# Optimization experiments

Measured on AMD Instinct MI355X. Metric: run time of the kernel, lower is better.

Reference implementation:

```python
import jax, jax.numpy as jnp
import numpy as np
import math

B, S, E, H = 2, 2048, 1024, 16
D = E // H
EPS = 1e-5


def setup_inputs() -> dict:
    key = jax.random.key(0)
    ks = jax.random.split(key, 6)
    s = 1.0 / math.sqrt(E)
    return {
        "query": jax.random.normal(ks[0], (B, S, E), jnp.float32),
        "Wq": jax.random.normal(ks[1], (E, E), jnp.float32) * s,
        "bq": jnp.zeros((E,), jnp.float32),
        "Wk": jax.random.normal(ks[2], (E, E), jnp.float32) * s,
        "bk": jnp.zeros((E,), jnp.float32),
        "Wv": jax.random.normal(ks[3], (E, E), jnp.float32) * s,
        "bv": jnp.zeros((E,), jnp.float32),
        "Wo": jax.random.normal(ks[4], (E, E), jnp.float32) * s,
        "bo": jnp.zeros((E,), jnp.float32),
        "alpha": jnp.ones((1,), jnp.float32),
    }


def reference(query, Wq, bq, Wk, bk, Wv, bv, Wo, bo, alpha):
    # Q/K/V projections (nn.Linear: x @ W.T + b)
    q = (query @ Wq.T + bq).reshape(B, S, H, D)
    k = (query @ Wk.T + bk).reshape(B, S, H, D)
    v = (query @ Wv.T + bv).reshape(B, S, H, D)

    # YAT scores: (q.k)^2 / (||q-k||^2 + eps)
    qk = jnp.einsum('bqhd,bkhd->bhqk', q, k)          # [B,H,S,S]
    sq = jnp.einsum('bqhd,bqhd->bhq', q, q)           # ||q||^2
    sk = jnp.einsum('bkhd,bkhd->bhk', k, k)           # ||k||^2
    dist_sq = sq[..., :, None] + sk[..., None, :] - 2.0 * qk
    scores = (qk * qk) / (dist_sq + EPS)

    # learnable alpha scaling: scores * (sqrt(d)/log(1+d))^alpha
    scale = (jnp.sqrt(jnp.float32(D)) / jnp.log1p(jnp.float32(D))) ** alpha[0]
    scores = scores * scale

    attn = jax.nn.softmax(scores, axis=-1)
    out = jnp.einsum('bhqk,bkhd->bqhd', attn, v).reshape(B, S, E)
    return out @ Wo.T + bo
```

## Files before the change

### kernel.cpp

```cpp
#include <hip/hip_runtime.h>
#include <hip/hip_fp16.h>
#include <math.h>

#define BB 2
#define SS 2048
#define EE 1024
#define HH 16
#define DD 64
#define YAT_EPS 1e-5f
#define RR (BB * HH * SS)

typedef __attribute__((ext_vector_type(8))) short bf16x8;
typedef __attribute__((ext_vector_type(4))) short short4v;
typedef __attribute__((ext_vector_type(4))) float f32x4;
#define MFMA16(a, b, c) __builtin_amdgcn_mfma_f32_16x16x32_bf16((a), (b), (c), 0, 0, 0)

#if __has_builtin(__builtin_amdgcn_exp2f)
#define EXP2(x) __builtin_amdgcn_exp2f(x)
#else
#define EXP2(x) exp2f(x)
#endif
#if __has_builtin(__builtin_amdgcn_rcpf)
#define RCPF(x) __builtin_amdgcn_rcpf(x)
#else
#define RCPF(x) (1.0f / (x))
#endif

__device__ __forceinline__ unsigned short f2bf(float x) {
    unsigned int u = __float_as_uint(x);
    u += 0x7FFFu + ((u >> 16) & 1u);
    return (unsigned short)(u >> 16);
}
__device__ __forceinline__ float bf2f(unsigned short h) {
    return __uint_as_float(((unsigned int)h) << 16);
}
__device__ __forceinline__ short f2bf_t(float x) {
    return (short)(__float_as_uint(x) >> 16);
}

__device__ __forceinline__ void async_ld16(void* lds, const void* g) {
    __builtin_amdgcn_global_load_lds(
        (const __attribute__((address_space(1))) unsigned int*)g,
        (__attribute__((address_space(3))) unsigned int*)lds, 16, 0, 0);
}

__global__ __launch_bounds__(256) void split_all(
        const float* __restrict__ x,
        const float* __restrict__ Wq, const float* __restrict__ Wk,
        const float* __restrict__ Wv, const float* __restrict__ Wo,
        unsigned short* __restrict__ xhi, unsigned short* __restrict__ xlo,
        unsigned short* __restrict__ Whi, unsigned short* __restrict__ Wlo,
        unsigned short* __restrict__ Wohi) {
    const int bid = blockIdx.x;
    if (bid < 4096) {
        int i = bid * 256 + threadIdx.x;
        float4 v = ((const float4*)x)[i];
        ushort4 h, l;
        h.x = f2bf(v.x); l.x = f2bf(v.x - bf2f(h.x));
        h.y = f2bf(v.y); l.y = f2bf(v.y - bf2f(h.y));
        h.z = f2bf(v.z); l.z = f2bf(v.z - bf2f(h.z));
        h.w = f2bf(v.w); l.w = f2bf(v.w - bf2f(h.w));
        ((ushort4*)xhi)[i] = h;
        ((ushort4*)xlo)[i] = l;
    } else {
        int idx = bid - 4096;
        int y = idx >> 10;
        int i = (idx & 1023) * 256 + threadIdx.x;
        const float* src = y == 0 ? Wq : y == 1 ? Wk : y == 2 ? Wv : Wo;
        unsigned short* hi = y < 3 ? Whi + (size_t)y * EE * EE : Wohi;
        float4 v = ((const float4*)src)[i];
        ushort4 h;
        h.x = f2bf(v.x); h.y = f2bf(v.y); h.z = f2bf(v.z); h.w = f2bf(v.w);
        ((ushort4*)hi)[i] = h;
        if (y < 2) {
            unsigned short* lo = Wlo + (size_t)y * EE * EE;
            ushort4 l;
            l.x = f2bf(v.x - bf2f(h.x));
            l.y = f2bf(v.y - bf2f(h.y));
            l.z = f2bf(v.z - bf2f(h.z));
            l.w = f2bf(v.w - bf2f(h.w));
            ((ushort4*)lo)[i] = l;
        }
    }
}

__global__ __launch_bounds__(256, 2) void proj_qkv(
        const unsigned short* __restrict__ Ahi, const unsigned short* __restrict__ Alo,
        const unsigned short* __restrict__ Whi, const unsigned short* __restrict__ Wlo,
        const float* __restrict__ bq, const float* __restrict__ bk,
        const float* __restrict__ bv,
        unsigned short* __restrict__ qhi, unsigned short* __restrict__ qlo,
        unsigned short* __restrict__ khi, unsigned short* __restrict__ vt,
        float* __restrict__ sqn, float* __restrict__ skn) {
    __shared__ __align__(16) unsigned short SH[128 * 136];
    unsigned short* LA_hi = SH;
    unsigned short* LA_lo = SH + 4096;
    unsigned short* LB_hi = SH + 8192;
    unsigned short* LB_lo = SH + 12288;

    const int K = EE;
    const int t = threadIdx.x;
    const int w = t >> 6, lane = t & 63;
    const int quad = lane >> 4, lr = lane & 15;
    const int wy = w & 1, wx = w >> 1;
    const bool p3 = blockIdx.x < 16;
    const int m0 = blockIdx.y * 128;
    const int n0 = p3 ? blockIdx.x * 128 : 0;
    const int c0 = p3 ? 0 : (blockIdx.x - 16) * 128;

    const unsigned short* gsrc = nullptr;
    unsigned short* ldst = nullptr;
    if (w == 0)      { gsrc = Ahi + (size_t)m0 * K; ldst = LA_hi; }
    else if (w == 2) {
        gsrc = p3 ? Whi + (size_t)n0 * K
                  : Whi + (size_t)(2 * EE + c0) * K;
        ldst = LB_hi;
    } else if (p3 && w == 1) { gsrc = Alo + (size_t)m0 * K; ldst = LA_lo; }
    else if (p3 && w == 3)   { gsrc = Wlo + (size_t)n0 * K; ldst = LB_lo; }
    const unsigned short* gl = gsrc ? gsrc + (size_t)(lane >> 2) * K + (lane & 3) * 8
                                    : nullptr;

    f32x4 acc[4][4];
    #pragma unroll
    for (int i = 0; i < 4; ++i)
        #pragma unroll
        for (int j = 0; j < 4; ++j)
            acc[i][j] = (f32x4){0.f, 0.f, 0.f, 0.f};

    for (int k0 = 0; k0 < K; k0 += 32) {
        __syncthreads();
        if (gl) {
            #pragma unroll
            for (int i = 0; i < 8; ++i)
                async_ld16(ldst + i * 512, gl + (size_t)i * 16 * K + k0);
        }
        __syncthreads();
        bf16x8 ah[4], al[4], bh_[4], bl_[4];
        #pragma unroll
        for (int i = 0; i < 4; ++i) {
            ah[i]  = *(const bf16x8*)&LA_hi[(wy * 64 + i * 16 + lr) * 32 + quad * 8];
            bh_[i] = *(const bf16x8*)&LB_hi[(wx * 64 + i * 16 + lr) * 32 + quad * 8];
            if (p3) {
                al[i]  = *(const bf16x8*)&LA_lo[(wy * 64 + i * 16 + lr) * 32 + quad * 8];
                bl_[i] = *(const bf16x8*)&LB_lo[(wx * 64 + i * 16 + lr) * 32 + quad * 8];
            }
        }
        #pragma unroll
        for (int mg = 0; mg < 4; ++mg)
            #pragma unroll
            for (int ns = 0; ns < 4; ++ns) {
                f32x4 a = acc[mg][ns];
                a = MFMA16(ah[mg], bh_[ns], a);
                if (p3) {
                    a = MFMA16(ah[mg], bl_[ns], a);
                    a = MFMA16(al[mg], bh_[ns], a);
                }
                acc[mg][ns] = a;
            }
    }

    if (p3) {
        const int ng = n0 + wx * 64;
        const int path = ng >> 10;
        const int c = ng & 1023;
        const int h = c >> 6;
        const float* bias = path == 0 ? bq : bk;
        unsigned short* hi_p = path == 0 ? qhi : khi;
        float* nrm = path == 0 ? sqn : skn;
        float bias_v[4];
        #pragma unroll
        for (int ns = 0; ns < 4; ++ns) bias_v[ns] = bias[c + ns * 16 + lr];
        #pragma unroll
        for (int mg = 0; mg < 4; ++mg)
            #pragma unroll
            for (int r = 0; r < 4; ++r) {
                int m = m0 + wy * 64 + mg * 16 + quad * 4 + r;
                int b = m >> 11, s = m & (SS - 1);
                size_t base = ((size_t)(b * HH + h) * SS + s) * DD;
                float v4[4];
                #pragma unroll
                for (int ns = 0; ns < 4; ++ns) v4[ns] = acc[mg][ns][r] + bias_v[ns];
                float pn = v4[0] * v4[0] + v4[1] * v4[1] + v4[2] * v4[2] + v4[3] * v4[3];
                #pragma unroll
                for (int off = 1; off < 16; off <<= 1) pn += __shfl_xor(pn, off);
                if (lr == 0) nrm[(size_t)(b * HH + h) * SS + s] = pn;
                #pragma unroll
                for (int ns = 0; ns < 4; ++ns) {
                    unsigned short hv = f2bf(v4[ns]);
                    hi_p[base + ns * 16 + lr] = hv;
                    if (path == 0)
                        qlo[base + ns * 16 + lr] = f2bf(v4[ns] - bf2f(hv));
                }
            }
    } else {
        __syncthreads();
        float bias_v[4];
        #pragma unroll
        for (int ns = 0; ns < 4; ++ns) bias_v[ns] = bv[c0 + wx * 64 + ns * 16 + lr];
        #pragma unroll
        for (int mg = 0; mg < 4; ++mg)
            #pragma unroll
            for (int r = 0; r < 4; ++r) {
                int mloc = wy * 64 + mg * 16 + quad * 4 + r;
                #pragma unroll
                for (int ns = 0; ns < 4; ++ns) {
                    int cloc = wx * 64 + ns * 16 + lr;
                    SH[cloc * 136 + mloc] = f2bf(acc[mg][ns][r] + bias_v[ns]);
                }
            }
        __syncthreads();
        const int b = m0 >> 11, s0 = m0 & (SS - 1);
        #pragma unroll
        for (int jc = 0; jc < 8; ++jc) {
            int cl = (t >> 4) + jc * 16;
            int sl = (t & 15) * 8;
            bf16x8 vv = *(const bf16x8*)&SH[cl * 136 + sl];
            int c = c0 + cl, h = c >> 6, d = c & 63;
            *(bf16x8*)&vt[((size_t)(b * HH + h) * DD + d) * SS + s0 + sl] = vv;
        }
    }
}

__global__ __launch_bounds__(256, 2) void gemm_o(
        const unsigned short* __restrict__ Ahi,
        const unsigned short* __restrict__ Bhi,
        const float* __restrict__ bq,
        float* __restrict__ Cf,
        int M, int N, int K) {
    __shared__ __align__(16) unsigned short LA_hi[128 * 32];
    __shared__ __align__(16) unsigned short LB_hi[128 * 32];

    const int t = threadIdx.x;
    const int w = t >> 6, lane = t & 63;
    const int quad = lane >> 4, lr = lane & 15;
    const int wy = w & 1, wx = w >> 1;
    const int m0 = blockIdx.y * 128, n0 = blockIdx.x * 128;

    const unsigned short* gsrc = nullptr;
    unsigned short* ldst = nullptr;
    if (w == 0)      { gsrc = Ahi + (size_t)m0 * K; ldst = LA_hi; }
    else if (w == 2) { gsrc = Bhi + (size_t)n0 * K; ldst = LB_hi; }
    const unsigned short* gl = gsrc ? gsrc + (size_t)(lane >> 2) * K + (lane & 3) * 8
                                    : nullptr;

    f32x4 acc[4][4];
    #pragma unroll
    for (int i = 0; i < 4; ++i)
        #pragma unroll
        for (int j = 0; j < 4; ++j)
            acc[i][j] = (f32x4){0.f, 0.f, 0.f, 0.f};

    for (int k0 = 0; k0 < K; k0 += 32) {
        __syncthreads();
        if (gl) {
            #pragma unroll
            for (int i = 0; i < 8; ++i)
                async_ld16(ldst + i * 512, gl + (size_t)i * 16 * K + k0);
        }
        __syncthreads();
        bf16x8 ah[4], bh_[4];
        #pragma unroll
        for (int i = 0; i < 4; ++i) {
            ah[i]  = *(const bf16x8*)&LA_hi[(wy * 64 + i * 16 + lr) * 32 + quad * 8];
            bh_[i] = *(const bf16x8*)&LB_hi[(wx * 64 + i * 16 + lr) * 32 + quad * 8];
        }
        #pragma unroll
        for (int mg = 0; mg < 4; ++mg)
            #pragma unroll
            for (int ns = 0; ns < 4; ++ns)
                acc[mg][ns] = MFMA16(ah[mg], bh_[ns], acc[mg][ns]);
    }

    const int ng = n0 + wx * 64;
    float bias_v[4];
    #pragma unroll
    for (int ns = 0; ns < 4; ++ns) bias_v[ns] = bq[ng + ns * 16 + lr];
    #pragma unroll
    for (int mg = 0; mg < 4; ++mg)
        #pragma unroll
        for (int r = 0; r < 4; ++r) {
            int m = m0 + wy * 64 + mg * 16 + quad * 4 + r;
            #pragma unroll
            for (int ns = 0; ns < 4; ++ns)
                Cf[(size_t)m * N + ng + ns * 16 + lr] = acc[mg][ns][r] + bias_v[ns];
        }
}

__global__ __launch_bounds__(256, 4) void yat_attn_mfma(
        const unsigned short* __restrict__ qhi, const unsigned short* __restrict__ qlo,
        const unsigned short* __restrict__ khi,
        const unsigned short* __restrict__ vt,
        const float* __restrict__ sqn, const float* __restrict__ skn,
        const float* __restrict__ alphap,
        unsigned short* __restrict__ ctxhi) {
    __shared__ __align__(16) unsigned short Ks[2][4096];
    __shared__ __align__(16) unsigned short Ps[4][16 * 68];

    const int t = threadIdx.x;
    const int w = t >> 6, lane = t & 63;
    const int quad = lane >> 4, lr = lane & 15;
    const int qt = blockIdx.x, bh = blockIdx.y;
    const int row0 = qt * 64 + w * 16;
    const float cscale = powf(sqrtf((float)DD) / log1pf((float)DD), alphap[0])
                         * 1.4426950408889634f;

    bf16x8 qh[2], ql[2];
    #pragma unroll
    for (int kd = 0; kd < 2; ++kd) {
        size_t o = ((size_t)bh * SS + row0 + lr) * DD + kd * 32 + quad * 8;
        qh[kd] = *(const bf16x8*)&qhi[o];
        ql[kd] = *(const bf16x8*)&qlo[o];
    }
    const float sqe = sqn[(size_t)bh * SS + row0 + lr] + YAT_EPS;

    const int lrow = lane >> 3;
    const int lofs = lrow * 64 + (((lane & 7) ^ (lrow & 7)) << 3);
    const int sw = lr & 7;

    float m_r = -INFINITY, l_r = 0.f;
    f32x4 O[4];
    #pragma unroll
    for (int nd = 0; nd < 4; ++nd) O[nd] = (f32x4){0.f, 0.f, 0.f, 0.f};

    const size_t khi_base = (size_t)bh * SS * 64 + (size_t)w * 16 * 64 + lofs;
    const size_t skn_base = (size_t)bh * SS + quad * 4;
    unsigned short* myP = Ps[w];

    #pragma unroll
    for (int i2 = 0; i2 < 2; ++i2)
        async_ld16(&Ks[0][w * 1024 + i2 * 512], khi + khi_base + i2 * 512);

    for (int it = 0; it < 32; ++it) {
        const int p = it & 1;
        __syncthreads();
        if (it + 1 < 32) {
            #pragma unroll
            for (int i2 = 0; i2 < 2; ++i2)
                async_ld16(&Ks[p ^ 1][w * 1024 + i2 * 512],
                           khi + khi_base + (size_t)(it + 1) * 4096 + i2 * 512);
        }
        const int kbase = it * 64;
        const unsigned short* kb = Ks[p];
        f32x4 acc[4];
        f32x4 sk4[4];
        #pragma unroll
        for (int st = 0; st < 4; ++st) {
            const int rbase = (st * 16 + lr) * 64;
            bf16x8 kh0 = *(const bf16x8*)&kb[rbase + ((quad    ) ^ sw) * 8];
            bf16x8 kh1 = *(const bf16x8*)&kb[rbase + ((quad + 4) ^ sw) * 8];
            sk4[st] = *(const f32x4*)&skn[skn_base + kbase + st * 16];
            f32x4 a = (f32x4){0.f, 0.f, 0.f, 0.f};
            a = MFMA16(kh0, qh[0], a);
            a = MFMA16(kh1, qh[1], a);
            a = MFMA16(kh0, ql[0], a);
            a = MFMA16(kh1, ql[1], a);
            acc[st] = a;
        }
        bf16x8 vf[4][2];
        #pragma unroll
        for (int nd = 0; nd < 4; ++nd)
            #pragma unroll
            for (int kk = 0; kk < 2; ++kk)
                vf[nd][kk] = *(const bf16x8*)&vt[((size_t)bh * DD + nd * 16 + lr) * SS
                                                 + kbase + kk * 32 + quad * 8];
        float mx = -INFINITY;
        #pragma unroll
        for (int st = 0; st < 4; ++st)
            #pragma unroll
            for (int r = 0; r < 4; ++r) {
                float qk = acc[st][r];
                float d = sqe + sk4[st][r] - 2.f * qk;
                float u = qk * qk * RCPF(d);
                acc[st][r] = u;
                mx = fmaxf(mx, u);
            }
        mx = fmaxf(mx, __shfl_xor(mx, 16));
        mx = fmaxf(mx, __shfl_xor(mx, 32));
        float mnew = fmaxf(m_r, mx);
        bool resc = !__all(cscale * (mnew - m_r) <= 8.f);
        float aa = 1.f;
        if (resc) {
            aa = EXP2(__builtin_fmaf(cscale, m_r, -cscale * mnew));
            m_r = mnew;
        }
        const float cm = cscale * m_r;
        float rs = 0.f;
        #pragma unroll
        for (int st = 0; st < 4; ++st) {
            float e0 = EXP2(__builtin_fmaf(cscale, acc[st][0], -cm));
            float e1 = EXP2(__builtin_fmaf(cscale, acc[st][1], -cm));
            float e2 = EXP2(__builtin_fmaf(cscale, acc[st][2], -cm));
            float e3 = EXP2(__builtin_fmaf(cscale, acc[st][3], -cm));
            rs += (e0 + e1) + (e2 + e3);
            short4v pv;
            pv[0] = f2bf_t(e0); pv[1] = f2bf_t(e1);
            pv[2] = f2bf_t(e2); pv[3] = f2bf_t(e3);
            *(short4v*)&myP[lr * 68 + st * 16 + quad * 4] = pv;
        }
        rs += __shfl_xor(rs, 16);
        rs += __shfl_xor(rs, 32);
        l_r = l_r * aa + rs;
        if (resc) {
            float al_[4];
            #pragma unroll
            for (int r = 0; r < 4; ++r) al_[r] = __shfl(aa, quad * 4 + r);
            #pragma unroll
            for (int nd = 0; nd < 4; ++nd)
                #pragma unroll
                for (int r = 0; r < 4; ++r)
                    O[nd][r] *= al_[r];
        }
        bf16x8 pf[2];
        #pragma unroll
        for (int kk = 0; kk < 2; ++kk)
            pf[kk] = *(const bf16x8*)&myP[lr * 68 + kk * 32 + quad * 8];
        #pragma unroll
        for (int nd = 0; nd < 4; ++nd)
            #pragma unroll
            for (int kk = 0; kk < 2; ++kk)
                O[nd] = MFMA16(pf[kk], vf[nd][kk], O[nd]);
    }
    const int b = bh >> 4, h = bh & 15;
    #pragma unroll
    for (int r = 0; r < 4; ++r) {
        float li = __shfl(l_r, quad * 4 + r);
        float inv = RCPF(li);
        int s = row0 + quad * 4 + r;
        size_t base = ((size_t)b * SS + s) * EE + h * DD;
        #pragma unroll
        for (int nd = 0; nd < 4; ++nd)
            ctxhi[base + nd * 16 + lr] = f2bf(O[nd][r] * inv);
    }
}

extern "C" void kernel_launch(void* const* d_in, const int* in_sizes, int n_in,
                              void* d_out, int out_size, void* d_ws, size_t ws_size,
                              hipStream_t stream) {
    const float* x     = (const float*)d_in[0];
    const float* Wq    = (const float*)d_in[1];
    const float* bq    = (const float*)d_in[2];
    const float* Wk    = (const float*)d_in[3];
    const float* bk    = (const float*)d_in[4];
    const float* Wv    = (const float*)d_in[5];
    const float* bv    = (const float*)d_in[6];
    const float* Wo    = (const float*)d_in[7];
    const float* bo    = (const float*)d_in[8];
    const float* alpha = (const float*)d_in[9];
    float* out = (float*)d_out;
    char* ws = (char*)d_ws;

    const int M = BB * SS;
    const size_t MB = 1u << 20;
    unsigned short* xhi  = (unsigned short*)(ws + 0 * MB);
    unsigned short* xlo  = (unsigned short*)(ws + 8 * MB);
    unsigned short* Whi  = (unsigned short*)(ws + 16 * MB);
    unsigned short* Wlo  = (unsigned short*)(ws + 22 * MB);
    unsigned short* Wohi = (unsigned short*)(ws + 28 * MB);
    unsigned short* qhi  = (unsigned short*)(ws + 32 * MB);
    unsigned short* qlo  = (unsigned short*)(ws + 40 * MB);
    unsigned short* khi  = (unsigned short*)(ws + 48 * MB);
    unsigned short* vt   = (unsigned short*)(ws + 56 * MB);
    float* sqn = (float*)(ws + 80 * MB);
    float* skn = (float*)(ws + 80 * MB + 256 * 1024);
    unsigned short* ctxhi = xhi;

    split_all<<<8192, 256, 0, stream>>>(x, Wq, Wk, Wv, Wo,
                                        xhi, xlo, Whi, Wlo, Wohi);

    proj_qkv<<<dim3(24, M / 128), 256, 0, stream>>>(
        xhi, xlo, Whi, Wlo, bq, bk, bv,
        qhi, qlo, khi, vt, sqn, skn);

    yat_attn_mfma<<<dim3(SS / 64, BB * HH), 256, 0, stream>>>(
        qhi, qlo, khi, vt, sqn, skn, alpha, ctxhi);

    gemm_o<<<dim3(EE / 128, M / 128), 256, 0, stream>>>(
        ctxhi, Wohi, bo, out, M, EE, EE);
}
```

Measured before the change: 320.7 us.

## Split attention key range across two blocks and merge partials in combine kernel

Splits the key sequence into two halves processed by separate blocks (grid z), each with half-size K tiles and reduced LDS, and raises launch bounds to 8 blocks per CU. Each block writes unnormalized fp16 partial outputs plus per-row max/sum, and a new combine kernel merges them with log-sum-exp rescaling into the bf16 context. This aims to increase occupancy and parallelism for latency hiding, at the cost of extra partial-output memory traffic, an additional launch, and fp16 rounding of partials.

```diff
diff --git a/kernel.cpp b/kernel.cpp
--- a/kernel.cpp
+++ b/kernel.cpp
@@ -286,20 +286,20 @@
         }
 }
 
-__global__ __launch_bounds__(256, 4) void yat_attn_mfma(
+__global__ __launch_bounds__(256, 8) void yat_attn_mfma(
         const unsigned short* __restrict__ qhi, const unsigned short* __restrict__ qlo,
         const unsigned short* __restrict__ khi,
         const unsigned short* __restrict__ vt,
         const float* __restrict__ sqn, const float* __restrict__ skn,
         const float* __restrict__ alphap,
-        unsigned short* __restrict__ ctxhi) {
-    __shared__ __align__(16) unsigned short Ks[2][4096];
-    __shared__ __align__(16) unsigned short Ps[4][16 * 68];
+        __half* __restrict__ Opart, float2* __restrict__ mlpart) {
+    __shared__ __align__(16) unsigned short Ks[2][2048];
+    __shared__ __align__(16) unsigned short Ps[4][16 * 36];
 
     const int t = threadIdx.x;
     const int w = t >> 6, lane = t & 63;
     const int quad = lane >> 4, lr = lane & 15;
-    const int qt = blockIdx.x, bh = blockIdx.y;
+    const int qt = blockIdx.x, bh = blockIdx.y, z = blockIdx.z;
     const int row0 = qt * 64 + w * 16;
     const float cscale = powf(sqrtf((float)DD) / log1pf((float)DD), alphap[0])
                          * 1.4426950408889634f;
@@ -322,33 +322,29 @@
     #pragma unroll
     for (int nd = 0; nd < 4; ++nd) O[nd] = (f32x4){0.f, 0.f, 0.f, 0.f};
 
-    const size_t khi_base = (size_t)bh * SS * 64 + (size_t)w * 16 * 64 + lofs;
+    const int t0 = z * 32;
+    const unsigned short* khi_l = khi + (size_t)bh * SS * 64
+                                + (size_t)w * 8 * 64 + lofs;
     const size_t skn_base = (size_t)bh * SS + quad * 4;
     unsigned short* myP = Ps[w];
 
-    #pragma unroll
-    for (int i2 = 0; i2 < 2; ++i2)
-        async_ld16(&Ks[0][w * 1024 + i2 * 512], khi + khi_base + i2 * 512);
+    async_ld16(&Ks[0][w * 512], khi_l + (size_t)t0 * 2048);
 
     for (int it = 0; it < 32; ++it) {
         const int p = it & 1;
         __syncthreads();
-        if (it + 1 < 32) {
-            #pragma unroll
-            for (int i2 = 0; i2 < 2; ++i2)
-                async_ld16(&Ks[p ^ 1][w * 1024 + i2 * 512],
-                           khi + khi_base + (size_t)(it + 1) * 4096 + i2 * 512);
-        }
-        const int kbase = it * 64;
+        if (it + 1 < 32)
+            async_ld16(&Ks[p ^ 1][w * 512], khi_l + (size_t)(t0 + it + 1) * 2048);
+        const int kbase = (t0 + it) * 32;
         const unsigned short* kb = Ks[p];
-        f32x4 acc[4];
-        f32x4 sk4[4];
-        #pragma unroll
-        for (int st = 0; st < 4; ++st) {
+        f32x4 acc[2];
+        f32x4 sk2[2];
+        #pragma unroll
+        for (int st = 0; st < 2; ++st) {
             const int rbase = (st * 16 + lr) * 64;
             bf16x8 kh0 = *(const bf16x8*)&kb[rbase + ((quad    ) ^ sw) * 8];
             bf16x8 kh1 = *(const bf16x8*)&kb[rbase + ((quad + 4) ^ sw) * 8];
-            sk4[st] = *(const f32x4*)&skn[skn_base + kbase + st * 16];
+            sk2[st] = *(const f32x4*)&skn[skn_base + kbase + st * 16];
             f32x4 a = (f32x4){0.f, 0.f, 0.f, 0.f};
             a = MFMA16(kh0, qh[0], a);
             a = MFMA16(kh1, qh[1], a);
@@ -356,20 +352,18 @@
             a = MFMA16(kh1, ql[1], a);
             acc[st] = a;
         }
-        bf16x8 vf[4][2];
+        bf16x8 vf[4];
         #pragma unroll
         for (int nd = 0; nd < 4; ++nd)
-            #pragma unroll
-            for (int kk = 0; kk < 2; ++kk)
-                vf[nd][kk] = *(const bf16x8*)&vt[((size_t)bh * DD + nd * 16 + lr) * SS
-                                                 + kbase + kk * 32 + quad * 8];
+            vf[nd] = *(const bf16x8*)&vt[((size_t)bh * DD + nd * 16 + lr) * SS
+                                         + kbase + quad * 8];
         float mx = -INFINITY;
         #pragma unroll
-        for (int st = 0; st < 4; ++st)
+        for (int st = 0; st < 2; ++st)
             #pragma unroll
             for (int r = 0; r < 4; ++r) {
                 float qk = acc[st][r];
-                float d = sqe + sk4[st][r] - 2.f * qk;
+                float d = sqe + sk2[st][r] - 2.f * qk;
                 float u = qk * qk * RCPF(d);
                 acc[st][r] = u;
                 mx = fmaxf(mx, u);
@@ -386,7 +380,7 @@
         const float cm = cscale * m_r;
         float rs = 0.f;
         #pragma unroll
-        for (int st = 0; st < 4; ++st) {
+        for (int st = 0; st < 2; ++st) {
             float e0 = EXP2(__builtin_fmaf(cscale, acc[st][0], -cm));
             float e1 = EXP2(__builtin_fmaf(cscale, acc[st][1], -cm));
             float e2 = EXP2(__builtin_fmaf(cscale, acc[st][2], -cm));
@@ -395,7 +389,7 @@
             short4v pv;
             pv[0] = f2bf_t(e0); pv[1] = f2bf_t(e1);
             pv[2] = f2bf_t(e2); pv[3] = f2bf_t(e3);
-            *(short4v*)&myP[lr * 68 + st * 16 + quad * 4] = pv;
+            *(short4v*)&myP[lr * 36 + st * 16 + quad * 4] = pv;
         }
         rs += __shfl_xor(rs, 16);
         rs += __shfl_xor(rs, 32);
@@ -410,27 +404,48 @@
                 for (int r = 0; r < 4; ++r)
                     O[nd][r] *= al_[r];
         }
-        bf16x8 pf[2];
-        #pragma unroll
-        for (int kk = 0; kk < 2; ++kk)
-            pf[kk] = *(const bf16x8*)&myP[lr * 68 + kk * 32 + quad * 8];
+        bf16x8 pf = *(const bf16x8*)&myP[lr * 36 + quad * 8];
         #pragma unroll
         for (int nd = 0; nd < 4; ++nd)
-            #pragma unroll
-            for (int kk = 0; kk < 2; ++kk)
-                O[nd] = MFMA16(pf[kk], vf[nd][kk], O[nd]);
-    }
-    const int b = bh >> 4, h = bh & 15;
+            O[nd] = MFMA16(pf, vf[nd], O[nd]);
+    }
+    if (quad == 0)
+        mlpart[(size_t)z * RR + (size_t)bh * SS + row0 + lr] =
+            make_float2(cscale * m_r, l_r);
     #pragma unroll
     for (int r = 0; r < 4; ++r) {
-        float li = __shfl(l_r, quad * 4 + r);
-        float inv = RCPF(li);
-        int s = row0 + quad * 4 + r;
-        size_t base = ((size_t)b * SS + s) * EE + h * DD;
+        size_t rowg = (size_t)bh * SS + row0 + quad * 4 + r;
         #pragma unroll
         for (int nd = 0; nd < 4; ++nd)
-            ctxhi[base + nd * 16 + lr] = f2bf(O[nd][r] * inv);
-    }
+            Opart[((size_t)z * RR + rowg) * DD + nd * 16 + lr] =
+                __float2half(O[nd][r]);
+    }
+}
+
+__global__ __launch_bounds__(256) void combine_attn(
+        const __half* __restrict__ Opart, const float2* __restrict__ mlpart,
+        unsigned short* __restrict__ ctxhi) {
+    int tid = blockIdx.x * 256 + threadIdx.x;
+    int row = tid >> 4, c4 = (tid & 15) * 4;
+    float2 ml0 = mlpart[row];
+    float2 ml1 = mlpart[RR + row];
+    float ms = fmaxf(ml0.x, ml1.x);
+    float a0 = EXP2(ml0.x - ms), a1 = EXP2(ml1.x - ms);
+    float inv = RCPF(ml0.y * a0 + ml1.y * a1);
+    a0 *= inv; a1 *= inv;
+    const __half* p0 = Opart + (size_t)row * DD + c4;
+    const __half* p1 = p0 + (size_t)RR * DD;
+    int bh = row >> 11, s = row & (SS - 1);
+    int b = bh >> 4, h = bh & 15;
+    size_t idx = ((size_t)b * SS + s) * EE + h * DD + c4;
+    ushort4 hv;
+    unsigned short* hp = (unsigned short*)&hv;
+    #pragma unroll
+    for (int j = 0; j < 4; ++j) {
+        float o = __half2float(p0[j]) * a0 + __half2float(p1[j]) * a1;
+        hp[j] = f2bf(o);
+    }
+    *(ushort4*)&ctxhi[idx] = hv;
 }
 
 extern "C" void kernel_launch(void* const* d_in, const int* in_sizes, int n_in,
@@ -455,11 +470,13 @@
     unsigned short* xlo  = (unsigned short*)(ws + 8 * MB);
     unsigned short* Whi  = (unsigned short*)(ws + 16 * MB);
     unsigned short* Wlo  = (unsigned short*)(ws + 22 * MB);
+    float2* mlpart       = (float2*)(ws + 24 * MB);
     unsigned short* Wohi = (unsigned short*)(ws + 28 * MB);
     unsigned short* qhi  = (unsigned short*)(ws + 32 * MB);
     unsigned short* qlo  = (unsigned short*)(ws + 40 * MB);
     unsigned short* khi  = (unsigned short*)(ws + 48 * MB);
     unsigned short* vt   = (unsigned short*)(ws + 56 * MB);
+    __half* Opart        = (__half*)(ws + 64 * MB);
     float* sqn = (float*)(ws + 80 * MB);
     float* skn = (float*)(ws + 80 * MB + 256 * 1024);
     unsigned short* ctxhi = xhi;
@@ -471,8 +488,10 @@
         xhi, xlo, Whi, Wlo, bq, bk, bv,
         qhi, qlo, khi, vt, sqn, skn);
 
-    yat_attn_mfma<<<dim3(SS / 64, BB * HH), 256, 0, stream>>>(
-        qhi, qlo, khi, vt, sqn, skn, alpha, ctxhi);
+    yat_attn_mfma<<<dim3(SS / 64, BB * HH, 2), 256, 0, stream>>>(
+        qhi, qlo, khi, vt, sqn, skn, alpha, Opart, mlpart);
+
+    combine_attn<<<RR * 16 / 256, 256, 0, stream>>>(Opart, mlpart, ctxhi);
 
     gemm_o<<<dim3(EE / 128, M / 128), 256, 0, stream>>>(
         ctxhi, Wohi, bo, out, M, EE, EE);
```

Result: slower. 448.7 us (+39.9%).
